# Optimization experiments

Hardware: AMD Instinct MI355X
Metric: run time of the kernel (lower is better)

The kernel has to match this reference:

```python
import jax, jax.numpy as jnp
import numpy as np

B, N_OBJ, N_VAL, E, H, HEADS = 512, 10, 200, 420, 128, 4
NPG = 1 + N_OBJ + N_VAL  # nodes per graph = 211
N = B * NPG
FMIN = float(np.finfo(np.float32).min)


def _gat_conv(x, src, dst, W, att_src, att_dst, bias, concat):
    # PyG GATConv (v1): linear (no bias) -> per-head attention logits ->
    # leaky_relu(a_src[j]+a_dst[i]) -> softmax over edges grouped by dst -> scatter-sum
    heads = att_src.shape[0]
    xs = (x @ W).reshape(N, heads, -1)            # [N, heads, C]
    a_src = (xs * att_src).sum(-1)                # [N, heads]
    a_dst = (xs * att_dst).sum(-1)                # [N, heads]
    alpha = jax.nn.leaky_relu(a_src[src] + a_dst[dst], 0.2)   # [Etot, heads]
    amax = jax.ops.segment_max(alpha, dst, num_segments=N)
    ex = jnp.exp(alpha - amax[dst])
    denom = jax.ops.segment_sum(ex, dst, num_segments=N)
    alpha = ex / (denom[dst] + 1e-16)
    out = jax.ops.segment_sum(xs[src] * alpha[..., None], dst, num_segments=N)  # [N,heads,C]
    out = out.reshape(N, -1) if concat else out.mean(axis=1)
    return out + bias


def setup_inputs() -> dict:
    key = jax.random.key(0)
    ks = jax.random.split(key, 24)
    s = 0.1
    C1 = H // HEADS  # 32
    inp = {
        'head_node': jax.random.normal(ks[0], (B, 2), jnp.float32),
        'objective_nodes': jax.random.normal(ks[1], (B, N_OBJ, 2), jnp.float32),
        'value_nodes': jax.random.normal(ks[2], (B, N_VAL, 5), jnp.float32),
        'edge_indices': jax.random.randint(ks[3], (B, 2, E), 0, NPG, jnp.int64 if jax.config.jax_enable_x64 else jnp.int32),
        'accept_mask': jnp.ones((B, 2), jnp.float32),
        'W_head': jax.random.normal(ks[4], (2, H)) * s, 'b_head': jnp.zeros((H,)),
        'W_obj': jax.random.normal(ks[5], (2, H)) * s, 'b_obj': jnp.zeros((H,)),
        'W_val': jax.random.normal(ks[6], (5, H)) * s, 'b_val': jnp.zeros((H,)),
        'W1': jax.random.normal(ks[7], (H, HEADS * C1)) * s,
        'att_src1': jax.random.normal(ks[8], (HEADS, C1)) * s,
        'att_dst1': jax.random.normal(ks[9], (HEADS, C1)) * s,
        'b1': jnp.zeros((HEADS * C1,)),
        'W2': jax.random.normal(ks[10], (H, HEADS * H)) * s,
        'att_src2': jax.random.normal(ks[11], (HEADS, H)) * s,
        'att_dst2': jax.random.normal(ks[12], (HEADS, H)) * s,
        'b2': jnp.zeros((H,)),
        'W_acc': jax.random.normal(ks[13], (H, 2)) * 0.01, 'b_acc': jnp.zeros((2,)),
        'W_off': jax.random.normal(ks[14], (H, 1)) * 0.01, 'b_off': jnp.zeros((1,)),
        'W_vf': jax.random.normal(ks[15], (H, 1)) * s, 'b_vf': jnp.zeros((1,)),
    }
    return inp


def reference(head_node, objective_nodes, value_nodes, edge_indices, accept_mask,
              W_head, b_head, W_obj, b_obj, W_val, b_val,
              W1, att_src1, att_dst1, b1, W2, att_src2, att_dst2, b2,
              W_acc, b_acc, W_off, b_off, W_vf, b_vf):
    # node encoders + ReLU
    h_head = jax.nn.relu(head_node @ W_head + b_head)                  # [B,H]
    h_obj = jax.nn.relu(objective_nodes @ W_obj + b_obj)               # [B,N_OBJ,H]
    h_val = jax.nn.relu(value_nodes @ W_val + b_val)                   # [B,N_VAL,H]
    h_nodes = jnp.concatenate([h_head[:, None], h_obj, h_val], axis=1)  # [B,NPG,H]
    x = h_nodes.reshape(N, H)
    # batch graphs: offset per-graph edge indices, add self loops
    offs = (jnp.arange(B, dtype=edge_indices.dtype) * NPG)[:, None, None]
    ei = (edge_indices + offs).transpose(1, 0, 2).reshape(2, -1)       # [2, B*E]
    loops = jnp.arange(N, dtype=edge_indices.dtype)
    src = jnp.concatenate([ei[0], loops])
    dst = jnp.concatenate([ei[1], loops])
    # GAT: layer1 concat heads, ReLU (BasicGNN inter-layer act), layer2 mean heads
    x1 = jax.nn.relu(_gat_conv(x, src, dst, W1, att_src1, att_dst1, b1, True))
    x2 = _gat_conv(x1, src, dst, W2, att_src2, att_dst2, b2, False)
    h_out = jax.nn.relu(x2).reshape(B, NPG, H)
    h_head_out = h_out[:, 0]                                           # [B,H]
    h_val_out = h_out[:, -N_VAL:]                                      # [B,N_VAL,H]
    offer_logits = (h_val_out @ W_off + b_off).squeeze(-1)             # [B,N_VAL]
    accept_inf_mask = jnp.maximum(jnp.log(accept_mask), FMIN)
    accept_logits = h_head_out @ W_acc + b_acc + accept_inf_mask       # [B,2]
    vf = h_head_out @ W_vf + b_vf                                      # [B,1]
    return jnp.concatenate([accept_logits, offer_logits, vf], axis=-1)  # [B, 2+N_VAL+1]
```

## Files before the change

kernel.cpp:

```cpp
#include <hip/hip_runtime.h>

typedef unsigned short u16;
typedef unsigned int u32;
typedef short short8 __attribute__((ext_vector_type(8)));
typedef float f32x4 __attribute__((ext_vector_type(4)));

#define NB   512
#define NPG  211
#define NOBJ 10
#define NVAL 200
#define NE   420
#define NN   (NB * NPG)

__device__ __forceinline__ float bf2f(u16 u){
  union { unsigned i; float f; } v; v.i = ((unsigned)u) << 16; return v.f;
}
__device__ __forceinline__ u16 f2bf(float f){
  union { float f; unsigned i; } v; v.f = f;
  return (u16)((v.i + 0x7FFFu + ((v.i >> 16) & 1u)) >> 16);
}
__device__ __forceinline__ float lo_bf(u32 u){ union{u32 i;float f;}v; v.i=u<<16; return v.f; }
__device__ __forceinline__ float hi_bf(u32 u){ union{u32 i;float f;}v; v.i=u&0xffff0000u; return v.f; }
__device__ __forceinline__ u32 pack_bf(float a, float b){ return (u32)f2bf(a) | ((u32)f2bf(b)<<16); }
__device__ __forceinline__ float lrelu(float s){ return s > 0.f ? s : 0.2f * s; }
__device__ __forceinline__ short8 pack8(ushort4 a, ushort4 b){
  short8 v;
  v[0]=(short)a.x; v[1]=(short)a.y; v[2]=(short)a.z; v[3]=(short)a.w;
  v[4]=(short)b.x; v[5]=(short)b.y; v[6]=(short)b.z; v[7]=(short)b.w;
  return v;
}
__device__ __forceinline__ int s16(int r, int c){
  return (r << 7) + ((((c >> 3) ^ (r & 15)) << 3) | (c & 7));
}

#define AS_GLOBAL(p) ((const __attribute__((address_space(1))) void*)((const void*)(p)))
#define AS_LDS(p)    ((__attribute__((address_space(3))) void*)((void*)(p)))

__global__ __launch_bounds__(256) void k_prep(const float* __restrict__ W1, const float* __restrict__ W2,
                                              const float* __restrict__ as2, const float* __restrict__ ad2,
                                              u16* __restrict__ W1t, u16* __restrict__ W2t,
                                              float* __restrict__ wms, float* __restrict__ wmd){
  int gid = blockIdx.x * 256 + threadIdx.x;
  if (gid < 16384){
    int k = gid >> 7, n = gid & 127;
    W1t[n * 128 + k] = f2bf(W1[k * 128 + n]);
  } else if (gid < 81920){
    int t = gid - 16384;
    int n = t >> 9, kk = t & 511;
    int h = kk >> 7, c = kk & 127;
    W2t[n * 512 + kk] = f2bf(W2[c * 512 + h * 128 + n]);
  } else {
    int t = gid - 81920;
    int which = t >> 9, hk = t & 511;
    int h = hk >> 7, k = hk & 127;
    const float* av = which ? ad2 : as2;
    float s = 0.f;
    for (int j = 0; j < 128; ++j)
      s += W2[k * 512 + h * 128 + j] * av[h * 128 + j];
    (which ? wmd : wms)[hk] = s;
  }
}

__global__ __launch_bounds__(256) void k_embed2(
    const float* __restrict__ head, const float* __restrict__ obj, const float* __restrict__ val,
    const float* __restrict__ Wh, const float* __restrict__ bh,
    const float* __restrict__ Wo, const float* __restrict__ bo,
    const float* __restrict__ Wv, const float* __restrict__ bv,
    u16* __restrict__ x){
  int gid = blockIdx.x * 256 + threadIdx.x;
  int n = gid >> 5, cc = (gid & 31) << 2;
  int g = n / NPG, loc = n - g * NPG;
  float a[4];
  if (loc == 0){
    const float* in = head + (size_t)g * 2;
    float i0 = in[0], i1 = in[1];
    #pragma unroll
    for (int t = 0; t < 4; ++t){ int c = cc + t; a[t] = bh[c] + i0 * Wh[c] + i1 * Wh[128 + c]; }
  } else if (loc <= NOBJ){
    const float* in = obj + ((size_t)g * NOBJ + (loc - 1)) * 2;
    float i0 = in[0], i1 = in[1];
    #pragma unroll
    for (int t = 0; t < 4; ++t){ int c = cc + t; a[t] = bo[c] + i0 * Wo[c] + i1 * Wo[128 + c]; }
  } else {
    const float* in = val + ((size_t)g * NVAL + (loc - 11)) * 5;
    float f[5];
    #pragma unroll
    for (int k = 0; k < 5; ++k) f[k] = in[k];
    #pragma unroll
    for (int t = 0; t < 4; ++t){
      int c = cc + t; float s = bv[c];
      #pragma unroll
      for (int k = 0; k < 5; ++k) s += f[k] * Wv[k * 128 + c];
      a[t] = s;
    }
  }
  ushort4 u;
  u.x = f2bf(fmaxf(a[0], 0.f)); u.y = f2bf(fmaxf(a[1], 0.f));
  u.z = f2bf(fmaxf(a[2], 0.f)); u.w = f2bf(fmaxf(a[3], 0.f));
  *(ushort4*)&x[(size_t)n * 128 + cc] = u;
}

__global__ __launch_bounds__(256) void k_csr2(const int* __restrict__ eidx,
                                              int* __restrict__ coff, int* __restrict__ csrc){
  __shared__ int sEs[420], sEd[420], sTmp[256], sOff[212], sSrc[632];
  int g = blockIdx.x, tid = threadIdx.x;
  const int4* e4 = (const int4*)(eidx + (size_t)g * 840);
  for (int i = tid; i < 105; i += 256){ ((int4*)sEs)[i] = e4[i]; ((int4*)sEd)[i] = e4[105 + i]; }
  __syncthreads();
  int deg = 0;
  if (tid < NPG){
    deg = 1;
    const int4* p4 = (const int4*)sEd;
    #pragma unroll 4
    for (int i = 0; i < 105; ++i){
      int4 v = p4[i];
      deg += (v.x == tid) + (v.y == tid) + (v.z == tid) + (v.w == tid);
    }
  }
  int v = deg;
  #pragma unroll
  for (int st = 1; st < 256; st <<= 1){
    sTmp[tid] = v;
    __syncthreads();
    if (tid >= st) v += sTmp[tid - st];
    __syncthreads();
  }
  if (tid < NPG) sOff[tid] = v - deg;
  if (tid == NPG - 1) sOff[NPG] = v;
  __syncthreads();
  if (tid < NPG){
    int p = sOff[tid];
    sSrc[p++] = tid;
    const int4* pd4 = (const int4*)sEd;
    const int4* ps4 = (const int4*)sEs;
    for (int i = 0; i < 105; ++i){
      int4 d = pd4[i]; int4 s = ps4[i];
      if (d.x == tid) sSrc[p++] = s.x;
      if (d.y == tid) sSrc[p++] = s.y;
      if (d.z == tid) sSrc[p++] = s.z;
      if (d.w == tid) sSrc[p++] = s.w;
    }
  }
  __syncthreads();
  if (tid < 212) coff[(size_t)g * 212 + tid] = sOff[tid];
  for (int i = tid; i < 631; i += 256) csrc[(size_t)g * 632 + i] = sSrc[i];
}

template<int KCH, bool RELU>
__global__ __launch_bounds__(512) void k_mm(const u16* __restrict__ A, int aStride, int chunkOff,
                                            const u16* __restrict__ Bt, int bstride,
                                            const float* __restrict__ bias, u16* __restrict__ C){
  __shared__ u16 sA[128 * 128];
  __shared__ u16 sB[128 * 128];
  const int tid = threadIdx.x, lane = tid & 63, w = tid >> 6;
  const int l15 = lane & 15, lg = lane >> 4;
  const int row0 = blockIdx.x * 128;
  f32x4 acc[8];
  #pragma unroll
  for (int ni = 0; ni < 8; ++ni) acc[ni] = (f32x4){0,0,0,0};

  #pragma unroll 1
  for (int ch = 0; ch < KCH; ++ch){
    const u16* Ab = A + (size_t)ch * chunkOff;
    const u16* Bb = Bt + ch * 128;
    #pragma unroll
    for (int i = 0; i < 4; ++i){
      int r = w * 16 + i * 4 + (lane >> 4);
      int c16 = lane & 15;
      int sw = (c16 ^ (r & 15)) << 4;
      __builtin_amdgcn_global_load_lds(AS_GLOBAL((const char*)(Ab + (size_t)(row0 + r) * aStride) + sw),
                                       AS_LDS(&sA[(w * 16 + i * 4) * 128]), 16, 0, 0);
      __builtin_amdgcn_global_load_lds(AS_GLOBAL((const char*)(Bb + (size_t)r * bstride) + sw),
                                       AS_LDS(&sB[(w * 16 + i * 4) * 128]), 16, 0, 0);
    }
    __syncthreads();
    #pragma unroll
    for (int kk = 0; kk < 4; ++kk){
      int k0 = kk * 32 + lg * 4;
      int rr = w * 16 + l15;
      short8 af = pack8(*(const ushort4*)&sA[s16(rr, k0)],
                        *(const ushort4*)&sA[s16(rr, k0 + 16)]);
      #pragma unroll
      for (int ni = 0; ni < 8; ++ni){
        int cc = ni * 16 + l15;
        short8 bf = pack8(*(const ushort4*)&sB[s16(cc, k0)],
                          *(const ushort4*)&sB[s16(cc, k0 + 16)]);
        acc[ni] = __builtin_amdgcn_mfma_f32_16x16x32_bf16(af, bf, acc[ni], 0, 0, 0);
      }
    }
    __syncthreads();
  }
  const int r0 = row0 + w * 16 + lg * 4;
  #pragma unroll
  for (int ni = 0; ni < 8; ++ni){
    int col = ni * 16 + l15;
    float bv = RELU ? bias[col] : 0.f;
    #pragma unroll
    for (int r = 0; r < 4; ++r){
      float v = acc[ni][r];
      if (RELU) v = fmaxf(v + bv, 0.f);
      C[(size_t)(r0 + r) * 128 + col] = f2bf(v);
    }
  }
}

__global__ __launch_bounds__(512) void k_attsm1(const u16* __restrict__ xs1,
                                                const float* __restrict__ as1, const float* __restrict__ ad1,
                                                const int* __restrict__ coff, const int* __restrict__ csrc,
                                                float* __restrict__ wn, float* __restrict__ rden){
  __shared__ float sLs[844], sLd[844];
  const int g = blockIdx.x, tid = threadIdx.x;
  const int gb = g * NPG;
  for (int t = tid; t < NPG * 4; t += 512){
    int n = t >> 2, h = t & 3;
    const u16* xr = xs1 + (size_t)(gb + n) * 128 + h * 32;
    float s = 0.f, d = 0.f;
    #pragma unroll
    for (int j = 0; j < 8; ++j){
      ushort4 xv = *(const ushort4*)(xr + j * 4);
      #pragma unroll
      for (int q = 0; q < 4; ++q){
        float xf = bf2f(((const u16*)&xv)[q]);
        int c = h * 32 + j * 4 + q;
        s += xf * as1[c];
        d += xf * ad1[c];
      }
    }
    sLs[t] = s; sLd[t] = d;
  }
  __syncthreads();
  for (int t = tid; t < NPG * 4; t += 512){
    int dst = t >> 2, h = t & 3;
    int o0 = coff[(size_t)g * 212 + dst], o1 = coff[(size_t)g * 212 + dst + 1];
    const int* sp = csrc + (size_t)g * 632;
    float ad = sLd[t];
    float m = -3e38f;
    for (int e = o0; e < o1; ++e) m = fmaxf(m, lrelu(sLs[sp[e] * 4 + h] + ad));
    float dn = 0.f;
    float* wp = wn + (size_t)g * 2528 + h * 632;
    for (int e = o0; e < o1; ++e){
      float ee = __expf(lrelu(sLs[sp[e] * 4 + h] + ad) - m);
      wp[e] = ee; dn += ee;
    }
    rden[(size_t)(gb + dst) * 4 + h] = 1.0f / (dn + 1e-16f);
  }
}

__global__ __launch_bounds__(512) void k_attsm2(const u16* __restrict__ x1,
                                                const float* __restrict__ wms, const float* __restrict__ wmd,
                                                const int* __restrict__ coff, const int* __restrict__ csrc,
                                                float* __restrict__ wn, float* __restrict__ rden){
  __shared__ float sw[1024];
  __shared__ float sLs[844], sLd[844];
  const int g = blockIdx.x, tid = threadIdx.x;
  const int gb = g * NPG;
  for (int i = tid; i < 1024; i += 512) sw[i] = (i < 512) ? wms[i] : wmd[i - 512];
  __syncthreads();
  for (int t = tid; t < NPG * 4; t += 512){
    int n = t >> 2, h = t & 3;
    const u16* xr = x1 + (size_t)(gb + n) * 128;
    const float* wsp = sw + h * 128;
    const float* wdp = sw + 512 + h * 128;
    float s = 0.f, d = 0.f;
    #pragma unroll
    for (int j = 0; j < 32; ++j){
      ushort4 xv = *(const ushort4*)(xr + j * 4);
      #pragma unroll
      for (int q = 0; q < 4; ++q){
        float xf = bf2f(((const u16*)&xv)[q]);
        s += xf * wsp[j * 4 + q];
        d += xf * wdp[j * 4 + q];
      }
    }
    sLs[t] = s; sLd[t] = d;
  }
  __syncthreads();
  for (int t = tid; t < NPG * 4; t += 512){
    int dst = t >> 2, h = t & 3;
    int o0 = coff[(size_t)g * 212 + dst], o1 = coff[(size_t)g * 212 + dst + 1];
    const int* sp = csrc + (size_t)g * 632;
    float ad = sLd[t];
    float m = -3e38f;
    for (int e = o0; e < o1; ++e) m = fmaxf(m, lrelu(sLs[sp[e] * 4 + h] + ad));
    float dn = 0.f;
    float* wp = wn + (size_t)g * 2528 + h * 632;
    for (int e = o0; e < o1; ++e){
      float ee = __expf(lrelu(sLs[sp[e] * 4 + h] + ad) - m);
      wp[e] = ee; dn += ee;
    }
    rden[(size_t)(gb + dst) * 4 + h] = 0.25f / (dn + 1e-16f);
  }
}

__global__ __launch_bounds__(256) void k_gat1k(const u16* __restrict__ xs1,
                                               const float* __restrict__ wn, const float* __restrict__ rden,
                                               const int* __restrict__ coff, const int* __restrict__ csrc,
                                               const float* __restrict__ b1, u16* __restrict__ x1){
  int bid = blockIdx.x;
  int g = bid / 53, ch = bid - g * 53;
  int dst = ch * 4 + (threadIdx.x >> 6);
  if (dst >= NPG) return;
  int lane = threadIdx.x & 63;
  int cp = lane << 1, hh = lane >> 4;
  int gb = g * NPG;
  int o0 = coff[(size_t)g * 212 + dst], o1 = coff[(size_t)g * 212 + dst + 1];
  const int* sp = csrc + (size_t)g * 632;
  const float* wp = wn + (size_t)g * 2528 + hh * 632;
  float a0 = 0.f, a1 = 0.f;
  for (int e = o0; e < o1; ++e){
    int src = sp[e];
    u32 f = *(const u32*)&xs1[(size_t)(gb + src) * 128 + cp];
    float w = wp[e];
    a0 += w * lo_bf(f); a1 += w * hi_bf(f);
  }
  float rv = rden[(size_t)(gb + dst) * 4 + hh];
  *(u32*)&x1[(size_t)(gb + dst) * 128 + cp] =
    pack_bf(fmaxf(a0 * rv + b1[cp], 0.f), fmaxf(a1 * rv + b1[cp + 1], 0.f));
}

__global__ __launch_bounds__(256) void k_gat2k(const u16* __restrict__ x1,
                                               const float* __restrict__ wn, const float* __restrict__ rden,
                                               const int* __restrict__ coff, const int* __restrict__ csrc,
                                               u16* __restrict__ y){
  int bid = blockIdx.x;
  int g = bid / 53, ch = bid - g * 53;
  int dst = ch * 4 + (threadIdx.x >> 6);
  if (dst >= NPG) return;
  int lane = threadIdx.x & 63;
  int cp = lane << 1;
  int gb = g * NPG;
  int o0 = coff[(size_t)g * 212 + dst], o1 = coff[(size_t)g * 212 + dst + 1];
  const int* sp = csrc + (size_t)g * 632;
  const float* wb = wn + (size_t)g * 2528;
  float a0[4] = {0,0,0,0}, a1[4] = {0,0,0,0};
  for (int e = o0; e < o1; ++e){
    int src = sp[e];
    u32 f = *(const u32*)&x1[(size_t)(gb + src) * 128 + cp];
    float xl = lo_bf(f), xh = hi_bf(f);
    #pragma unroll
    for (int h = 0; h < 4; ++h){
      float w = wb[h * 632 + e];
      a0[h] += w * xl; a1[h] += w * xh;
    }
  }
  u16* yr = y + (size_t)(gb + dst) * 512;
  #pragma unroll
  for (int h = 0; h < 4; ++h){
    float rv = rden[(size_t)(gb + dst) * 4 + h];
    *(u32*)&yr[h * 128 + cp] = pack_bf(a0[h] * rv, a1[h] * rv);
  }
}

__global__ __launch_bounds__(256) void k_final2(const u16* __restrict__ out2, const float* __restrict__ amask,
                                                const float* __restrict__ Wacc, const float* __restrict__ bacc,
                                                const float* __restrict__ Woff, const float* __restrict__ boff,
                                                const float* __restrict__ Wvf,  const float* __restrict__ bvf,
                                                float* __restrict__ out){
  int g = blockIdx.x >> 2;
  int t = ((blockIdx.x & 3) << 8) + threadIdx.x;
  if (t >= 812) return;
  int o = t >> 2, q = t & 3;
  float s = 0.f;
  if (o < 200){
    const u16* row = out2 + (size_t)(g * NPG + 11 + o) * 128;
    #pragma unroll
    for (int j = 0; j < 8; ++j){
      int c = q * 32 + j * 4;
      ushort4 xv = *(const ushort4*)(row + c);
      s += bf2f(xv.x)*Woff[c] + bf2f(xv.y)*Woff[c+1] + bf2f(xv.z)*Woff[c+2] + bf2f(xv.w)*Woff[c+3];
    }
  } else if (o < 202){
    int j2 = o - 200;
    const u16* row = out2 + (size_t)(g * NPG) * 128;
    #pragma unroll
    for (int j = 0; j < 8; ++j){
      int c = q * 32 + j * 4;
      ushort4 xv = *(const ushort4*)(row + c);
      s += bf2f(xv.x)*Wacc[c*2+j2] + bf2f(xv.y)*Wacc[(c+1)*2+j2]
         + bf2f(xv.z)*Wacc[(c+2)*2+j2] + bf2f(xv.w)*Wacc[(c+3)*2+j2];
    }
  } else {
    const u16* row = out2 + (size_t)(g * NPG) * 128;
    #pragma unroll
    for (int j = 0; j < 8; ++j){
      int c = q * 32 + j * 4;
      ushort4 xv = *(const ushort4*)(row + c);
      s += bf2f(xv.x)*Wvf[c] + bf2f(xv.y)*Wvf[c+1] + bf2f(xv.z)*Wvf[c+2] + bf2f(xv.w)*Wvf[c+3];
    }
  }
  s += __shfl_xor(s, 1);
  s += __shfl_xor(s, 2);
  if (q == 0){
    if (o < 200){
      out[(size_t)g * 203 + 2 + o] = s + boff[0];
    } else if (o < 202){
      int j2 = o - 200;
      float lm = logf(amask[g * 2 + j2]);
      out[(size_t)g * 203 + j2] = s + bacc[j2] + fmaxf(lm, -3.402823466e38f);
    } else {
      out[(size_t)g * 203 + 202] = s + bvf[0];
    }
  }
}

extern "C" void kernel_launch(void* const* d_in, const int* in_sizes, int n_in,
                              void* d_out, int out_size, void* d_ws, size_t ws_size,
                              hipStream_t stream){
  (void)in_sizes; (void)n_in; (void)out_size; (void)ws_size;
  const float* head = (const float*)d_in[0];
  const float* obj  = (const float*)d_in[1];
  const float* val  = (const float*)d_in[2];
  const int*   eidx = (const int*)d_in[3];
  const float* amask= (const float*)d_in[4];
  const float* Wh   = (const float*)d_in[5];
  const float* bh   = (const float*)d_in[6];
  const float* Wo   = (const float*)d_in[7];
  const float* bo   = (const float*)d_in[8];
  const float* Wv   = (const float*)d_in[9];
  const float* bv   = (const float*)d_in[10];
  const float* W1   = (const float*)d_in[11];
  const float* as1  = (const float*)d_in[12];
  const float* ad1  = (const float*)d_in[13];
  const float* b1   = (const float*)d_in[14];
  const float* W2   = (const float*)d_in[15];
  const float* as2  = (const float*)d_in[16];
  const float* ad2  = (const float*)d_in[17];
  const float* b2   = (const float*)d_in[18];
  const float* Wacc = (const float*)d_in[19];
  const float* bacc = (const float*)d_in[20];
  const float* Woff = (const float*)d_in[21];
  const float* boff = (const float*)d_in[22];
  const float* Wvf  = (const float*)d_in[23];
  const float* bvf  = (const float*)d_in[24];
  float* out = (float*)d_out;

  char* ws = (char*)d_ws;
  u16*   W1t = (u16*)ws;
  u16*   W2t = (u16*)(ws + 32768);
  float* wms = (float*)(ws + 163840);
  float* wmd = (float*)(ws + 165888);
  int*   coff = (int*)(ws + 167936);
  int*   csrc = (int*)(ws + 602112);
  float* wn   = (float*)(ws + 5353472);
  float* rden = (float*)(ws + 10530816);
  u16*   x    = (u16*)(ws + 12259328);
  u16*   xs1  = (u16*)(ws + 39915520);
  u16*   y    = (u16*)(ws + 67571712);

  k_prep<<<324, 256, 0, stream>>>(W1, W2, as2, ad2, W1t, W2t, wms, wmd);
  k_embed2<<<NN * 32 / 256, 256, 0, stream>>>(head, obj, val, Wh, bh, Wo, bo, Wv, bv, x);
  k_csr2<<<NB, 256, 0, stream>>>(eidx, coff, csrc);
  k_mm<1, false><<<NN / 128, 512, 0, stream>>>(x, 128, 0, W1t, 128, nullptr, xs1);
  k_attsm1<<<NB, 512, 0, stream>>>(xs1, as1, ad1, coff, csrc, wn, rden);
  k_gat1k<<<NB * 53, 256, 0, stream>>>(xs1, wn, rden, coff, csrc, b1, x);
  k_attsm2<<<NB, 512, 0, stream>>>(x, wms, wmd, coff, csrc, wn, rden);
  k_gat2k<<<NB * 53, 256, 0, stream>>>(x, wn, rden, coff, csrc, y);
  k_mm<4, true><<<NN / 128, 512, 0, stream>>>(y, 512, 128, W2t, 512, b2, xs1);
  k_final2<<<NB * 4, 256, 0, stream>>>(xs1, amask, Wacc, bacc, Woff, boff, Wvf, bvf, out);
}
```

Baseline: 262.2 us.

## Reorder GAT layer-2 as transform-then-aggregate, fuse output heads, skip unused nodes

```diff
diff --git a/kernel.cpp b/kernel.cpp
--- a/kernel.cpp
+++ b/kernel.cpp
@@ -39,7 +39,8 @@
 __global__ __launch_bounds__(256) void k_prep(const float* __restrict__ W1, const float* __restrict__ W2,
                                               const float* __restrict__ as2, const float* __restrict__ ad2,
                                               u16* __restrict__ W1t, u16* __restrict__ W2t,
-                                              float* __restrict__ wms, float* __restrict__ wmd){
+                                              float* __restrict__ wms, float* __restrict__ wmd,
+                                              u16* __restrict__ W2z){
   int gid = blockIdx.x * 256 + threadIdx.x;
   if (gid < 16384){
     int k = gid >> 7, n = gid & 127;
@@ -49,7 +50,7 @@
     int n = t >> 9, kk = t & 511;
     int h = kk >> 7, c = kk & 127;
     W2t[n * 512 + kk] = f2bf(W2[c * 512 + h * 128 + n]);
-  } else {
+  } else if (gid < 82944){
     int t = gid - 81920;
     int which = t >> 9, hk = t & 511;
     int h = hk >> 7, k = hk & 127;
@@ -58,6 +59,10 @@
     for (int j = 0; j < 128; ++j)
       s += W2[k * 512 + h * 128 + j] * av[h * 128 + j];
     (which ? wmd : wms)[hk] = s;
+  } else {
+    int t = gid - 82944;
+    int c = t >> 7, k = t & 127;
+    W2z[c * 128 + k] = f2bf(W2[k * 512 + c]);
   }
 }
 
@@ -201,6 +206,55 @@
       if (RELU) v = fmaxf(v + bv, 0.f);
       C[(size_t)(r0 + r) * 128 + col] = f2bf(v);
     }
+  }
+}
+
+__global__ __launch_bounds__(512) void k_mmz(const u16* __restrict__ A,
+                                             const u16* __restrict__ W2z,
+                                             u16* __restrict__ z){
+  __shared__ u16 sA[128 * 128];
+  __shared__ u16 sB[128 * 128];
+  const int tid = threadIdx.x, lane = tid & 63, w = tid >> 6;
+  const int l15 = lane & 15, lg = lane >> 4;
+  const int row0 = (blockIdx.x >> 2) * 128;
+  const int cy   = blockIdx.x & 3;
+  const u16* Bb = W2z + cy * 16384;
+  f32x4 acc[8];
+  #pragma unroll
+  for (int ni = 0; ni < 8; ++ni) acc[ni] = (f32x4){0,0,0,0};
+
+  #pragma unroll
+  for (int i = 0; i < 4; ++i){
+    int r = w * 16 + i * 4 + (lane >> 4);
+    int c16 = lane & 15;
+    int sw = (c16 ^ (r & 15)) << 4;
+    __builtin_amdgcn_global_load_lds(AS_GLOBAL((const char*)(A + (size_t)(row0 + r) * 128) + sw),
+                                     AS_LDS(&sA[(w * 16 + i * 4) * 128]), 16, 0, 0);
+    __builtin_amdgcn_global_load_lds(AS_GLOBAL((const char*)(Bb + (size_t)r * 128) + sw),
+                                     AS_LDS(&sB[(w * 16 + i * 4) * 128]), 16, 0, 0);
+  }
+  __syncthreads();
+  #pragma unroll
+  for (int kk = 0; kk < 4; ++kk){
+    int k0 = kk * 32 + lg * 4;
+    int rr = w * 16 + l15;
+    short8 af = pack8(*(const ushort4*)&sA[s16(rr, k0)],
+                      *(const ushort4*)&sA[s16(rr, k0 + 16)]);
+    #pragma unroll
+    for (int ni = 0; ni < 8; ++ni){
+      int cc = ni * 16 + l15;
+      short8 bf = pack8(*(const ushort4*)&sB[s16(cc, k0)],
+                        *(const ushort4*)&sB[s16(cc, k0 + 16)]);
+      acc[ni] = __builtin_amdgcn_mfma_f32_16x16x32_bf16(af, bf, acc[ni], 0, 0, 0);
+    }
+  }
+  const int r0 = row0 + w * 16 + lg * 4;
+  #pragma unroll
+  for (int ni = 0; ni < 8; ++ni){
+    int col = cy * 128 + ni * 16 + l15;
+    #pragma unroll
+    for (int r = 0; r < 4; ++r)
+      z[(size_t)(r0 + r) * 512 + col] = f2bf(acc[ni][r]);
   }
 }
 
@@ -318,88 +372,64 @@
     pack_bf(fmaxf(a0 * rv + b1[cp], 0.f), fmaxf(a1 * rv + b1[cp + 1], 0.f));
 }
 
-__global__ __launch_bounds__(256) void k_gat2k(const u16* __restrict__ x1,
-                                               const float* __restrict__ wn, const float* __restrict__ rden,
-                                               const int* __restrict__ coff, const int* __restrict__ csrc,
-                                               u16* __restrict__ y){
+__global__ __launch_bounds__(256) void k_aggp(const u16* __restrict__ z,
+                                              const float* __restrict__ wn, const float* __restrict__ rden,
+                                              const int* __restrict__ coff, const int* __restrict__ csrc,
+                                              const float* __restrict__ b2, const float* __restrict__ amask,
+                                              const float* __restrict__ Wacc, const float* __restrict__ bacc,
+                                              const float* __restrict__ Woff, const float* __restrict__ boff,
+                                              const float* __restrict__ Wvf,  const float* __restrict__ bvf,
+                                              float* __restrict__ out){
   int bid = blockIdx.x;
-  int g = bid / 53, ch = bid - g * 53;
-  int dst = ch * 4 + (threadIdx.x >> 6);
-  if (dst >= NPG) return;
+  int g = bid / 51, chunk = bid - g * 51;
+  int idx = chunk * 4 + (threadIdx.x >> 6);
+  if (idx >= 201) return;
+  int dst = (idx == 0) ? 0 : 10 + idx;
   int lane = threadIdx.x & 63;
   int cp = lane << 1;
   int gb = g * NPG;
   int o0 = coff[(size_t)g * 212 + dst], o1 = coff[(size_t)g * 212 + dst + 1];
   const int* sp = csrc + (size_t)g * 632;
   const float* wb = wn + (size_t)g * 2528;
-  float a0[4] = {0,0,0,0}, a1[4] = {0,0,0,0};
+  float a00 = 0, a01 = 0, a10 = 0, a11 = 0, a20 = 0, a21 = 0, a30 = 0, a31 = 0;
   for (int e = o0; e < o1; ++e){
     int src = sp[e];
-    u32 f = *(const u32*)&x1[(size_t)(gb + src) * 128 + cp];
-    float xl = lo_bf(f), xh = hi_bf(f);
-    #pragma unroll
-    for (int h = 0; h < 4; ++h){
-      float w = wb[h * 632 + e];
-      a0[h] += w * xl; a1[h] += w * xh;
-    }
-  }
-  u16* yr = y + (size_t)(gb + dst) * 512;
-  #pragma unroll
-  for (int h = 0; h < 4; ++h){
-    float rv = rden[(size_t)(gb + dst) * 4 + h];
-    *(u32*)&yr[h * 128 + cp] = pack_bf(a0[h] * rv, a1[h] * rv);
-  }
-}
-
-__global__ __launch_bounds__(256) void k_final2(const u16* __restrict__ out2, const float* __restrict__ amask,
-                                                const float* __restrict__ Wacc, const float* __restrict__ bacc,
-                                                const float* __restrict__ Woff, const float* __restrict__ boff,
-                                                const float* __restrict__ Wvf,  const float* __restrict__ bvf,
-                                                float* __restrict__ out){
-  int g = blockIdx.x >> 2;
-  int t = ((blockIdx.x & 3) << 8) + threadIdx.x;
-  if (t >= 812) return;
-  int o = t >> 2, q = t & 3;
-  float s = 0.f;
-  if (o < 200){
-    const u16* row = out2 + (size_t)(g * NPG + 11 + o) * 128;
-    #pragma unroll
-    for (int j = 0; j < 8; ++j){
-      int c = q * 32 + j * 4;
-      ushort4 xv = *(const ushort4*)(row + c);
-      s += bf2f(xv.x)*Woff[c] + bf2f(xv.y)*Woff[c+1] + bf2f(xv.z)*Woff[c+2] + bf2f(xv.w)*Woff[c+3];
-    }
-  } else if (o < 202){
-    int j2 = o - 200;
-    const u16* row = out2 + (size_t)(g * NPG) * 128;
-    #pragma unroll
-    for (int j = 0; j < 8; ++j){
-      int c = q * 32 + j * 4;
-      ushort4 xv = *(const ushort4*)(row + c);
-      s += bf2f(xv.x)*Wacc[c*2+j2] + bf2f(xv.y)*Wacc[(c+1)*2+j2]
-         + bf2f(xv.z)*Wacc[(c+2)*2+j2] + bf2f(xv.w)*Wacc[(c+3)*2+j2];
+    const u16* zr = z + (size_t)(gb + src) * 512 + cp;
+    u32 f0 = *(const u32*)&zr[0];
+    u32 f1 = *(const u32*)&zr[128];
+    u32 f2 = *(const u32*)&zr[256];
+    u32 f3 = *(const u32*)&zr[384];
+    float w0 = wb[e], w1 = wb[632 + e], w2 = wb[1264 + e], w3 = wb[1896 + e];
+    a00 += w0 * lo_bf(f0); a01 += w0 * hi_bf(f0);
+    a10 += w1 * lo_bf(f1); a11 += w1 * hi_bf(f1);
+    a20 += w2 * lo_bf(f2); a21 += w2 * hi_bf(f2);
+    a30 += w3 * lo_bf(f3); a31 += w3 * hi_bf(f3);
+  }
+  float4 rv = *(const float4*)&rden[(size_t)(gb + dst) * 4];
+  float o2a = fmaxf(b2[cp]     + rv.x * a00 + rv.y * a10 + rv.z * a20 + rv.w * a30, 0.f);
+  float o2b = fmaxf(b2[cp + 1] + rv.x * a01 + rv.y * a11 + rv.z * a21 + rv.w * a31, 0.f);
+  if (idx == 0){
+    float pA0 = o2a * Wacc[cp * 2]     + o2b * Wacc[(cp + 1) * 2];
+    float pA1 = o2a * Wacc[cp * 2 + 1] + o2b * Wacc[(cp + 1) * 2 + 1];
+    float pV  = o2a * Wvf[cp]          + o2b * Wvf[cp + 1];
+    #pragma unroll
+    for (int s = 1; s < 64; s <<= 1){
+      pA0 += __shfl_xor(pA0, s);
+      pA1 += __shfl_xor(pA1, s);
+      pV  += __shfl_xor(pV, s);
+    }
+    if (lane == 0){
+      float lm0 = fmaxf(logf(amask[g * 2]),     -3.402823466e38f);
+      float lm1 = fmaxf(logf(amask[g * 2 + 1]), -3.402823466e38f);
+      out[(size_t)g * 203]       = pA0 + bacc[0] + lm0;
+      out[(size_t)g * 203 + 1]   = pA1 + bacc[1] + lm1;
+      out[(size_t)g * 203 + 202] = pV + bvf[0];
     }
   } else {
-    const u16* row = out2 + (size_t)(g * NPG) * 128;
-    #pragma unroll
-    for (int j = 0; j < 8; ++j){
-      int c = q * 32 + j * 4;
-      ushort4 xv = *(const ushort4*)(row + c);
-      s += bf2f(xv.x)*Wvf[c] + bf2f(xv.y)*Wvf[c+1] + bf2f(xv.z)*Wvf[c+2] + bf2f(xv.w)*Wvf[c+3];
-    }
-  }
-  s += __shfl_xor(s, 1);
-  s += __shfl_xor(s, 2);
-  if (q == 0){
-    if (o < 200){
-      out[(size_t)g * 203 + 2 + o] = s + boff[0];
-    } else if (o < 202){
-      int j2 = o - 200;
-      float lm = logf(amask[g * 2 + j2]);
-      out[(size_t)g * 203 + j2] = s + bacc[j2] + fmaxf(lm, -3.402823466e38f);
-    } else {
-      out[(size_t)g * 203 + 202] = s + bvf[0];
-    }
+    float pO = o2a * Woff[cp] + o2b * Woff[cp + 1];
+    #pragma unroll
+    for (int s = 1; s < 64; s <<= 1) pO += __shfl_xor(pO, s);
+    if (lane == 0) out[(size_t)g * 203 + 2 + (idx - 1)] = pO + boff[0];
   }
 }
 
@@ -441,20 +471,21 @@
   float* wmd = (float*)(ws + 165888);
   int*   coff = (int*)(ws + 167936);
   int*   csrc = (int*)(ws + 602112);
+  u16*   W2z  = (u16*)(ws + 1896448);
   float* wn   = (float*)(ws + 5353472);
   float* rden = (float*)(ws + 10530816);
   u16*   x    = (u16*)(ws + 12259328);
   u16*   xs1  = (u16*)(ws + 39915520);
-  u16*   y    = (u16*)(ws + 67571712);
-
-  k_prep<<<324, 256, 0, stream>>>(W1, W2, as2, ad2, W1t, W2t, wms, wmd);
+  u16*   z    = (u16*)(ws + 67571712);
+
+  k_prep<<<580, 256, 0, stream>>>(W1, W2, as2, ad2, W1t, W2t, wms, wmd, W2z);
   k_embed2<<<NN * 32 / 256, 256, 0, stream>>>(head, obj, val, Wh, bh, Wo, bo, Wv, bv, x);
   k_csr2<<<NB, 256, 0, stream>>>(eidx, coff, csrc);
   k_mm<1, false><<<NN / 128, 512, 0, stream>>>(x, 128, 0, W1t, 128, nullptr, xs1);
   k_attsm1<<<NB, 512, 0, stream>>>(xs1, as1, ad1, coff, csrc, wn, rden);
   k_gat1k<<<NB * 53, 256, 0, stream>>>(xs1, wn, rden, coff, csrc, b1, x);
   k_attsm2<<<NB, 512, 0, stream>>>(x, wms, wmd, coff, csrc, wn, rden);
-  k_gat2k<<<NB * 53, 256, 0, stream>>>(x, wn, rden, coff, csrc, y);
-  k_mm<4, true><<<NN / 128, 512, 0, stream>>>(y, 512, 128, W2t, 512, b2, xs1);
-  k_final2<<<NB * 4, 256, 0, stream>>>(xs1, amask, Wacc, bacc, Woff, boff, Wvf, bvf, out);
-}
+  k_mmz<<<(NN / 128) * 4, 512, 0, stream>>>(x, W2z, z);
+  k_aggp<<<NB * 51, 256, 0, stream>>>(z, wn, rden, coff, csrc, b2, amask,
+                                      Wacc, bacc, Woff, boff, Wvf, bvf, out);
+}
```

New measurement: 253.8 us. 1.03x faster.
